# Kernel tuning notes

Measured on AMD Instinct MI355X. Metric: run time of the kernel, lower is better.

Reference implementation:

```python
import jax, jax.numpy as jnp
import numpy as np

K_TOP = 16
TEMP = 1.0
EPS = 1e-9

def setup_inputs() -> dict:
    key = jax.random.key(0)
    k1, k2, k3 = jax.random.split(key, 3)
    B, H, N, D = 4, 8, 2048, 64
    q = jax.random.normal(k1, (B, H, N, D), dtype=jnp.float32)
    k = jax.random.normal(k2, (B, H, N, D), dtype=jnp.float32)
    u = jax.random.uniform(k3, (B, N, N), dtype=jnp.float32)
    return {"q": q, "k": k, "u": u}

def reference(q, k, u):
    # q, k: [B, H, N, D]; u: uniform noise [B, N, N]
    d_head = q.shape[-1]
    scale = 1.0 / jnp.sqrt(jnp.asarray(d_head, dtype=q.dtype))
    # [B, H, N, N] scores, then mean over heads -> [B, N, N]
    attn_scores = jnp.einsum('bhnd,bhmd->bhnm', q, k) * scale
    logits = attn_scores.mean(axis=1)
    gumbel = -jnp.log(-jnp.log(u + EPS) + EPS)
    probs = jax.nn.softmax((logits + gumbel) / TEMP, axis=-1)
    topk_vals = jax.lax.top_k(probs, K_TOP)[0]          # [B, N, K]
    thresh = topk_vals.min(axis=-1, keepdims=True)      # [B, N, 1]
    sparse_mask = (probs >= thresh).astype(probs.dtype)
    return sparse_mask[:, None, :, :]                   # [B, 1, N, N]
```

## Files before the change

kernel.cpp:

```cpp
#include <hip/hip_runtime.h>
#include <math.h>

#define BB 4
#define HH 8
#define NN 2048
#define DD 64
#define KTOP 16
#define CUT_MARGIN 1e-3f

typedef _Float16 half_t;
typedef __attribute__((ext_vector_type(8))) _Float16 half8;
typedef __attribute__((ext_vector_type(4))) float floatx4;

__device__ __forceinline__ void gl_lds16(const half_t* g, half_t* l) {
    __builtin_amdgcn_global_load_lds(
        (const __attribute__((address_space(1))) void*)g,
        (__attribute__((address_space(3))) void*)l, 16, 0, 0);
}

__global__ __launch_bounds__(256) void split_swz(const float* __restrict__ q,
                                                 const float* __restrict__ kk,
                                                 half_t* __restrict__ qhi,
                                                 half_t* __restrict__ qlo,
                                                 half_t* __restrict__ khi,
                                                 half_t* __restrict__ klo) {
    const int uidx = blockIdx.x * 256 + threadIdx.x;
    const int row  = uidx >> 3;
    const int kg   = uidx & 7;
    const size_t src = (size_t)uidx * 8;
    const size_t dst = (size_t)row * 64 + (size_t)((kg ^ (row & 7)) << 3);

    float a[8], b[8];
    *(float4*)&a[0] = *(const float4*)(q + src);
    *(float4*)&a[4] = *(const float4*)(q + src + 4);
    *(float4*)&b[0] = *(const float4*)(kk + src);
    *(float4*)&b[4] = *(const float4*)(kk + src + 4);
    half8 qh, ql, kh, kl;
#pragma unroll
    for (int e = 0; e < 8; ++e) {
        half_t hq = (half_t)a[e];
        half_t hk = (half_t)b[e];
        qh[e] = hq; ql[e] = (half_t)((a[e] - (float)hq) * 2048.0f);
        kh[e] = hk; kl[e] = (half_t)((b[e] - (float)hk) * 2048.0f);
    }
    *(half8*)(qhi + dst) = qh;
    *(half8*)(qlo + dst) = ql;
    *(half8*)(khi + dst) = kh;
    *(half8*)(klo + dst) = kl;
}

__global__ __launch_bounds__(256, 2) void gemm_f16x3(const half_t* __restrict__ qhi,
                                                     const half_t* __restrict__ qlo,
                                                     const half_t* __restrict__ khi,
                                                     const half_t* __restrict__ klo,
                                                     float* __restrict__ L) {
    const int b  = blockIdx.z;
    const int i0 = blockIdx.y * 128;
    const int j0 = blockIdx.x * 128;
    const int tid  = threadIdx.x;
    const int wave = __builtin_amdgcn_readfirstlane(tid >> 6);
    const int lane = tid & 63;
    const int wr = wave >> 1, wc = wave & 1;
    const int lm = lane & 15, quad = lane >> 4;

    __shared__ __align__(16) half_t Ah[128 * 64];
    __shared__ __align__(16) half_t Al[128 * 64];
    __shared__ __align__(16) half_t Bh[128 * 64];
    __shared__ __align__(16) half_t Bl[128 * 64];

    const int off0 = (lane >> 3) * 64 + (lane & 7) * 8;

    floatx4 acc1[4][4], acc2[4][4];
#pragma unroll
    for (int tr = 0; tr < 4; ++tr)
#pragma unroll
        for (int tc = 0; tc < 4; ++tc) {
            acc1[tr][tc] = (floatx4)0.0f;
            acc2[tr][tc] = (floatx4)0.0f;
        }

    for (int h = 0; h < HH; ++h) {
        const size_t aoff = ((size_t)(b * HH + h) * NN + i0) * DD;
        const size_t boff = ((size_t)(b * HH + h) * NN + j0) * DD;
        const half_t* gbase;
        half_t* lbase;
        if      (wave == 0) { gbase = qhi + aoff; lbase = Ah; }
        else if (wave == 1) { gbase = qlo + aoff; lbase = Al; }
        else if (wave == 2) { gbase = khi + boff; lbase = Bh; }
        else                { gbase = klo + boff; lbase = Bl; }
        gbase += off0;

        __syncthreads();
#pragma unroll
        for (int i = 0; i < 16; ++i)
            gl_lds16(gbase + i * 512, lbase + i * 512);
        __syncthreads();

#pragma unroll
        for (int ks = 0; ks < 2; ++ks) {
            half8 ah[4], al[4], bh[4], bl[4];
            const int unit = ks * 4 + quad;
#pragma unroll
            for (int t = 0; t < 4; ++t) {
                const int am = wr * 64 + t * 16 + lm;
                const int bm = wc * 64 + t * 16 + lm;
                const int ai = am * 64 + ((unit ^ (am & 7)) << 3);
                const int bi = bm * 64 + ((unit ^ (bm & 7)) << 3);
                ah[t] = *(const half8*)&Ah[ai];
                al[t] = *(const half8*)&Al[ai];
                bh[t] = *(const half8*)&Bh[bi];
                bl[t] = *(const half8*)&Bl[bi];
            }
#pragma unroll
            for (int tr = 0; tr < 4; ++tr)
#pragma unroll
                for (int tc = 0; tc < 4; ++tc) {
                    acc1[tr][tc] = __builtin_amdgcn_mfma_f32_16x16x32_f16(
                        ah[tr], bh[tc], acc1[tr][tc], 0, 0, 0);
                    acc2[tr][tc] = __builtin_amdgcn_mfma_f32_16x16x32_f16(
                        ah[tr], bl[tc], acc2[tr][tc], 0, 0, 0);
                    acc2[tr][tc] = __builtin_amdgcn_mfma_f32_16x16x32_f16(
                        al[tr], bh[tc], acc2[tr][tc], 0, 0, 0);
                }
        }
    }

    const float s1 = 0.015625f;
    const float s2 = 0.015625f / 2048.0f;
#pragma unroll
    for (int tr = 0; tr < 4; ++tr)
#pragma unroll
        for (int r = 0; r < 4; ++r) {
            const int grow = i0 + wr * 64 + tr * 16 + quad * 4 + r;
            float* Lp = L + ((size_t)b * NN + grow) * NN + j0 + wc * 64 + lm;
#pragma unroll
            for (int tc = 0; tc < 4; ++tc)
                Lp[tc * 16] = acc1[tr][tc][r] * s1 + acc2[tr][tc][r] * s2;
        }
}

__device__ __forceinline__ unsigned long long flip64(double x) {
    unsigned long long v = (unsigned long long)__double_as_longlong(x);
    return v ^ ((0ULL - (v >> 63)) | 0x8000000000000000ULL);
}
__device__ __forceinline__ double unflip64(unsigned long long k) {
    unsigned long long v = (k >> 63) ? (k ^ 0x8000000000000000ULL) : ~k;
    return __longlong_as_double((long long)v);
}

__global__ __launch_bounds__(256, 3) void topk_mask(float* __restrict__ LM,
                                                    const float* __restrict__ u) {
    const int wave = threadIdx.x >> 6, lane = threadIdx.x & 63;
    const int row = blockIdx.x * 4 + wave;
    float* lrow = LM + (size_t)row * NN;
    const float* urow = u + (size_t)row * NN;

    __shared__ int   s_idx[4][64];
    __shared__ float s_L[4][64];

    float4 lv4[8], uv4[8];
#pragma unroll
    for (int e = 0; e < 8; ++e) lv4[e] = *(const float4*)(lrow + e * 256 + lane * 4);
#pragma unroll
    for (int e = 0; e < 8; ++e) uv4[e] = *(const float4*)(urow + e * 256 + lane * 4);

    float z[32];
#pragma unroll
    for (int e = 0; e < 8; ++e) {
        const float* us = (const float*)&uv4[e];
        const float* ls = (const float*)&lv4[e];
#pragma unroll
        for (int s = 0; s < 4; ++s) {
            float w = -__logf(us[s] + 1e-9f);
            z[e * 4 + s] = ls[s] - __logf(w + 1e-9f);
        }
    }

    float v = z[0];
#pragma unroll
    for (int r = 1; r < 32; ++r) v = fmaxf(v, z[r]);
#pragma unroll
    for (int kS = 2; kS <= 64; kS <<= 1) {
#pragma unroll
        for (int j = kS >> 1; j > 0; j >>= 1) {
            float o = __shfl_xor(v, j, 64);
            bool asc = ((lane & kS) == 0);
            bool lower = ((lane & j) == 0);
            float mn = fminf(v, o), mx = fmaxf(v, o);
            v = (asc == lower) ? mn : mx;
        }
    }
    const float cut = __shfl(v, 48, 64) - CUT_MARGIN;

    int c = 0;
#pragma unroll
    for (int r = 0; r < 32; ++r) {
        bool p = (z[r] >= cut);
        unsigned long long m = __ballot(p);
        if (p) {
            int slot = c + __popcll(m & ((1ULL << lane) - 1ULL));
            if (slot < 64) {
                s_idx[wave][slot] = (r >> 2) * 256 + lane * 4 + (r & 3);
                s_L[wave][slot]   = ((const float*)&lv4[r >> 2])[r & 3];
            }
        }
        c += __popcll(m);
    }
    if (c > 64) c = 64;

    unsigned long long key = 0xFFFFFFFFFFFFFFFFULL;
    if (lane < c) {
        int idx = s_idx[wave][lane];
        double uu = (double)urow[idx] + 1e-9;
        double w  = -log(uu);
        double g  = -log(w + 1e-9);
        key = flip64((double)s_L[wave][lane] + g);
    }
    const int rounds = c - (KTOP - 1);
    unsigned long long m = 0;
    for (int r = 0; r < rounds; ++r) {
        m = key;
#pragma unroll
        for (int off = 32; off >= 1; off >>= 1) {
            unsigned long long o = __shfl_xor(m, off, 64);
            m = (o < m) ? o : m;
        }
        unsigned long long bm = __ballot(key == m);
        if (lane == __builtin_ctzll(bm)) key = 0xFFFFFFFFFFFFFFFFULL;
    }
    const double thresh = unflip64(m);

    const float t_hi = (float)thresh + 3e-4f;
    const float t_lo = (float)thresh - 3e-4f;
#pragma unroll
    for (int e = 0; e < 8; ++e) {
        float o[4];
#pragma unroll
        for (int s = 0; s < 4; ++s) {
            const float uu32 = ((const float*)&uv4[e])[s];
            const float zz = z[e * 4 + s];
            const bool hardu = (uu32 > 0.999f);
            float val;
            if (!hardu && zz > t_hi)      val = 1.0f;
            else if (!hardu && zz < t_lo) val = 0.0f;
            else {
                double uu = (double)uu32 + 1e-9;
                double w  = -log(uu);
                double g  = -log(w + 1e-9);
                double z64 = (double)((const float*)&lv4[e])[s] + g;
                val = (z64 >= thresh) ? 1.0f : 0.0f;
            }
            o[s] = val;
        }
        *(float4*)(lrow + e * 256 + lane * 4) = *(float4*)o;
    }
}

extern "C" void kernel_launch(void* const* d_in, const int* in_sizes, int n_in,
                              void* d_out, int out_size, void* d_ws, size_t ws_size,
                              hipStream_t stream) {
    const float* q = (const float*)d_in[0];
    const float* k = (const float*)d_in[1];
    const float* u = (const float*)d_in[2];
    float* out = (float*)d_out;
    const size_t NQ = (size_t)BB * HH * NN * DD;
    half_t* qhi = (half_t*)d_ws;
    half_t* qlo = qhi + NQ;
    half_t* khi = qlo + NQ;
    half_t* klo = khi + NQ;

    split_swz<<<(int)(NQ / 8 / 256), 256, 0, stream>>>(q, k, qhi, qlo, khi, klo);

    dim3 grid1(NN / 128, NN / 128, BB);
    gemm_f16x3<<<grid1, 256, 0, stream>>>(qhi, qlo, khi, klo, out);

    topk_mask<<<(BB * NN) / 4, 256, 0, stream>>>(out, u);
}
```

Baseline: 228.2 us.

## Cut topk_mask register footprint with one-wave blocks and streamed row loads

```diff
diff --git a/kernel.cpp b/kernel.cpp
--- a/kernel.cpp
+++ b/kernel.cpp
@@ -148,32 +148,35 @@
     return __longlong_as_double((long long)v);
 }
 
-__global__ __launch_bounds__(256, 3) void topk_mask(float* __restrict__ LM,
-                                                    const float* __restrict__ u) {
-    const int wave = threadIdx.x >> 6, lane = threadIdx.x & 63;
-    const int row = blockIdx.x * 4 + wave;
+__global__ __launch_bounds__(64) void topk_mask(float* __restrict__ LM,
+                                                const float* __restrict__ u) {
+    const int row  = blockIdx.x;
+    const int lane = threadIdx.x;
     float* lrow = LM + (size_t)row * NN;
     const float* urow = u + (size_t)row * NN;
 
-    __shared__ int   s_idx[4][64];
-    __shared__ float s_L[4][64];
-
-    float4 lv4[8], uv4[8];
-#pragma unroll
-    for (int e = 0; e < 8; ++e) lv4[e] = *(const float4*)(lrow + e * 256 + lane * 4);
-#pragma unroll
-    for (int e = 0; e < 8; ++e) uv4[e] = *(const float4*)(urow + e * 256 + lane * 4);
+    __shared__ int s_idx[64];
 
     float z[32];
+    unsigned hard = 0;
+    float4 lb = *(const float4*)(lrow + lane * 4);
+    float4 ub = *(const float4*)(urow + lane * 4);
 #pragma unroll
     for (int e = 0; e < 8; ++e) {
-        const float* us = (const float*)&uv4[e];
-        const float* ls = (const float*)&lv4[e];
+        float4 lnx, unx;
+        if (e < 7) {
+            lnx = *(const float4*)(lrow + (e + 1) * 256 + lane * 4);
+            unx = *(const float4*)(urow + (e + 1) * 256 + lane * 4);
+        }
+        const float* ls = (const float*)&lb;
+        const float* us = (const float*)&ub;
 #pragma unroll
         for (int s = 0; s < 4; ++s) {
             float w = -__logf(us[s] + 1e-9f);
             z[e * 4 + s] = ls[s] - __logf(w + 1e-9f);
-        }
+            hard |= (us[s] > 0.999f ? 1u : 0u) << (e * 4 + s);
+        }
+        lb = lnx; ub = unx;
     }
 
     float v = z[0];
@@ -199,10 +202,7 @@
         unsigned long long m = __ballot(p);
         if (p) {
             int slot = c + __popcll(m & ((1ULL << lane) - 1ULL));
-            if (slot < 64) {
-                s_idx[wave][slot] = (r >> 2) * 256 + lane * 4 + (r & 3);
-                s_L[wave][slot]   = ((const float*)&lv4[r >> 2])[r & 3];
-            }
+            if (slot < 64) s_idx[slot] = (r >> 2) * 256 + lane * 4 + (r & 3);
         }
         c += __popcll(m);
     }
@@ -210,11 +210,11 @@
 
     unsigned long long key = 0xFFFFFFFFFFFFFFFFULL;
     if (lane < c) {
-        int idx = s_idx[wave][lane];
+        int idx = s_idx[lane];
         double uu = (double)urow[idx] + 1e-9;
         double w  = -log(uu);
         double g  = -log(w + 1e-9);
-        key = flip64((double)s_L[wave][lane] + g);
+        key = flip64((double)lrow[idx] + g);
     }
     const int rounds = c - (KTOP - 1);
     unsigned long long m = 0;
@@ -237,17 +237,18 @@
         float o[4];
 #pragma unroll
         for (int s = 0; s < 4; ++s) {
-            const float uu32 = ((const float*)&uv4[e])[s];
-            const float zz = z[e * 4 + s];
-            const bool hardu = (uu32 > 0.999f);
+            const int t = e * 4 + s;
+            const float zz = z[t];
+            const bool hardb = (hard >> t) & 1u;
             float val;
-            if (!hardu && zz > t_hi)      val = 1.0f;
-            else if (!hardu && zz < t_lo) val = 0.0f;
+            if (!hardb && zz > t_hi)      val = 1.0f;
+            else if (!hardb && zz < t_lo) val = 0.0f;
             else {
-                double uu = (double)uu32 + 1e-9;
+                const int idx = e * 256 + lane * 4 + s;
+                double uu = (double)urow[idx] + 1e-9;
                 double w  = -log(uu);
                 double g  = -log(w + 1e-9);
-                double z64 = (double)((const float*)&lv4[e])[s] + g;
+                double z64 = (double)lrow[idx] + g;
                 val = (z64 >= thresh) ? 1.0f : 0.0f;
             }
             o[s] = val;
@@ -274,5 +275,5 @@
     dim3 grid1(NN / 128, NN / 128, BB);
     gemm_f16x3<<<grid1, 256, 0, stream>>>(qhi, qlo, khi, klo, out);
 
-    topk_mask<<<(BB * NN) / 4, 256, 0, stream>>>(out, u);
-}
+    topk_mask<<<BB * NN, 64, 0, stream>>>(out, u);
+}
```

Result: no change. 224.7 us (-1.5%).
